# Kernel tuning notes

Measured on AMD Instinct MI355X. Metric: run time of the kernel, lower is better.

The kernel has to match this reference:

```python
import jax, jax.numpy as jnp
import numpy as np

B, N, D, H = 4, 8192, 1024, 16
C = D // H  # head dim = 64
EPS = 1e-6


def setup_inputs() -> dict:
    key = jax.random.key(0)
    ks = jax.random.split(key, 8)
    sc = 0.02
    return {
        "q": jax.random.normal(ks[0], (B, N, D), jnp.float32),
        "k": jax.random.normal(ks[1], (B, N, D), jnp.float32),
        "v": jax.random.normal(ks[2], (B, N, D), jnp.float32),
        "Wq": jax.random.normal(ks[3], (D, D), jnp.float32) * sc,
        "Wk": jax.random.normal(ks[4], (D, D), jnp.float32) * sc,
        "Wv": jax.random.normal(ks[5], (D, D), jnp.float32) * sc,
        "Wproj": jax.random.normal(ks[6], (D, D), jnp.float32) * sc,
        "focusing_factor": jnp.asarray(3.0, jnp.float32),
    }


def _to_heads(x):
    # b n (h c) -> (b h) n c
    return x.reshape(B, N, H, C).transpose(0, 2, 1, 3).reshape(B * H, N, C)


def reference(q, k, v, Wq, Wk, Wv, Wproj, focusing_factor):
    # projections (torch Linear: x @ W.T, no bias)
    qp = q @ Wq.T
    kp = k @ Wk.T
    vp = v @ Wv.T

    def feature_map(x):
        # |GELU(x)| + eps, then focused renormalization:
        # softmax(focusing_factor * log(f)) * mean(f)
        f = jnp.abs(jax.nn.gelu(x, approximate=False)) + EPS
        f_norm = f.mean(axis=-1, keepdims=True)
        return jax.nn.softmax(jnp.log(f) * focusing_factor, axis=-1) * f_norm

    qf = feature_map(qp)
    kf = feature_map(kp)

    qh = _to_heads(qf)  # [B*H, N, C]
    kh = _to_heads(kf)
    vh = _to_heads(vp)

    k_mean = kh.mean(axis=1)  # [B*H, C]
    z_inv = jnp.einsum('bnd,bd->bn', qh, k_mean) + EPS  # [B*H, N]

    # (k/sqrt(N))^T (v/sqrt(N)) == (k^T v)/N
    kv = jnp.einsum('bnc,bnd->bcd', kh, vh) / N  # [B*H, C, C]
    y = jnp.einsum('bic,bcd->bid', qh, kv) / z_inv[..., None]  # [B*H, N, C]

    y = y.reshape(B, H, N, C).transpose(0, 2, 1, 3).reshape(B, N, D)
    return y @ Wproj.T
```

## Files before the change

kernel.cpp:

```cpp
#include <hip/hip_runtime.h>

using f16 = _Float16;
typedef __attribute__((ext_vector_type(4))) _Float16 f16x4;
typedef __attribute__((ext_vector_type(8))) _Float16 f16x8;
typedef __attribute__((ext_vector_type(4))) float f32x4;

#define DEVI __device__ __forceinline__

namespace {

constexpr int BB = 4;
constexpr int NN = 8192;
constexpr int DD = 1024;
constexpr int MTOT = BB * NN;
constexpr float FSCALE = 64.0f;
constexpr float ZCONST = 64.0f * 64.0f * (8192.0f * 1e-6f);

DEVI void gl16(const void* g, void* l) {
  __builtin_amdgcn_global_load_lds(
      (__attribute__((address_space(1))) void*)(void*)g,
      (__attribute__((address_space(3))) void*)l, 16, 0, 0);
}

DEVI float wsum(float v) {
#pragma unroll
  for (int m = 32; m > 0; m >>= 1) v += __shfl_xor(v, m, 64);
  return v;
}

struct CastArgs {
  const float* src[8];
  f16* dst[8];
  int n4[8];
};

__global__ __launch_bounds__(256) void cast_kernel(CastArgs a) {
  const int z = blockIdx.y;
  const float4* __restrict__ s = (const float4*)a.src[z];
  f16x4* __restrict__ d = (f16x4*)a.dst[z];
  const int n4 = a.n4[z];
  for (int i = blockIdx.x * blockDim.x + threadIdx.x; i < n4;
       i += gridDim.x * blockDim.x) {
    float4 f = s[i];
    f16x4 o = {(f16)f.x, (f16)f.y, (f16)f.z, (f16)f.w};
    d[i] = o;
  }
}

struct Gemm3 {
  const f16* A[3];
  const f16* Bt[3];
  void* C[3];
};
struct Gemm3f {
  const float* A[3];
  const f16* Bt[3];
  f16* C[3];
};

#define GEMM_PREAMBLE()                                                      \
  constexpr int K = DD;                                                      \
  constexpr int N = DD;                                                      \
  constexpr int NKT = K / 64;                                                \
  const int nx = gridDim.x;                                                  \
  int lin = blockIdx.y * nx + blockIdx.x;                                    \
  const int cpx = (gridDim.y * nx) >> 3;                                     \
  lin = (lin & 7) * cpx + (lin >> 3);                                        \
  const size_t row0 = (size_t)(lin / nx) * 256;                              \
  const size_t col0 = (size_t)(lin % nx) * 256;                              \
  const int tid = threadIdx.x, lane = tid & 63, wv = tid >> 6;               \
  const int wm = wv >> 2, wn = wv & 3;                                       \
  const int fr = lane & 15, f7 = lane & 7, kq = lane >> 4;                   \
  const int srow = wv * 8 + (lane >> 3);                                     \
  const int ssw = (lane & 7) ^ ((lane >> 3) & 7);                            \
  const int c0e = (kq ^ f7) * 8;

__global__ __launch_bounds__(512, 2) void gemm256_fa(Gemm3f P) {
  GEMM_PREAMBLE()
  const int z = blockIdx.z;
  const float* __restrict__ A = P.A[z];
  const f16* __restrict__ Bt = P.Bt[z];
  f16* __restrict__ C = P.C[z];

  __shared__ __align__(16) f16 LA[2][2][8192];
  __shared__ __align__(16) f16 LB[2][2][8192];

  auto stageB = [&](int kts, int half) {
    const f16* src = Bt + (col0 + half * 128 + srow) * K + kts * 64 + ssw * 8;
    f16* dst = &LB[kts & 1][half][wv * 512];
#pragma unroll
    for (int c = 0; c < 2; ++c) gl16(src + (size_t)c * 64 * K, dst + c * 4096);
  };

  const int ar = tid >> 2;
  const int ac2 = (tid & 3) * 2;
  auto loadA = [&](int kts, float4* r) {
#pragma unroll
    for (int half = 0; half < 2; ++half) {
      const float* src = A + (row0 + half * 128 + ar) * (size_t)K + kts * 64;
#pragma unroll
      for (int c = 0; c < 2; ++c) {
        r[half * 4 + 2 * c + 0] = *(const float4*)(src + (ac2 + c) * 8);
        r[half * 4 + 2 * c + 1] = *(const float4*)(src + (ac2 + c) * 8 + 4);
      }
    }
  };
  auto writeA = [&](int kts, const float4* r) {
#pragma unroll
    for (int half = 0; half < 2; ++half) {
      f16* base = &LA[kts & 1][half][ar * 64];
#pragma unroll
      for (int c = 0; c < 2; ++c) {
        const float4 lo = r[half * 4 + 2 * c], hi = r[half * 4 + 2 * c + 1];
        f16x8 o = {(f16)lo.x, (f16)lo.y, (f16)lo.z, (f16)lo.w,
                   (f16)hi.x, (f16)hi.y, (f16)hi.z, (f16)hi.w};
        *(f16x8*)&base[((ac2 + c) ^ (ar & 7)) * 8] = o;
      }
    }
  };

  f32x4 acc[8][4];
#pragma unroll
  for (int i = 0; i < 8; ++i)
#pragma unroll
    for (int j = 0; j < 4; ++j) acc[i][j] = f32x4{0.f, 0.f, 0.f, 0.f};

  float4 ra[8];
  loadA(0, ra);
  stageB(0, 0); stageB(0, 1);
  asm volatile("s_waitcnt vmcnt(0)" ::: "memory");
  writeA(0, ra);
  asm volatile("s_waitcnt lgkmcnt(0)" ::: "memory");
  loadA(1, ra);
  __builtin_amdgcn_s_barrier();

  for (int kt = 0; kt < NKT; ++kt) {
    const int buf = kt & 1;
    const f16* Ah = LA[buf][wm];
    const f16* Bh = &LB[buf][wn >> 1][(wn & 1) * 4096];
    f16x8 a0[8], a1[8], b0[4], b1[4];

#pragma unroll
    for (int mi = 0; mi < 8; ++mi)
      a0[mi] = *(const f16x8*)&Ah[(mi * 16 + fr) * 64 + c0e];
#pragma unroll
    for (int ni = 0; ni < 4; ++ni)
      b0[ni] = *(const f16x8*)&Bh[(ni * 16 + fr) * 64 + c0e];
    if (kt + 1 < NKT) stageB(kt + 1, 0);
    __builtin_amdgcn_s_barrier();
    asm volatile("s_waitcnt lgkmcnt(0)" ::: "memory");
    __builtin_amdgcn_sched_barrier(0);
    __builtin_amdgcn_s_setprio(1);
#pragma unroll
    for (int mi = 0; mi < 4; ++mi)
#pragma unroll
      for (int ni = 0; ni < 4; ++ni)
        acc[mi][ni] = __builtin_amdgcn_mfma_f32_16x16x32_f16(
            a0[mi], b0[ni], acc[mi][ni], 0, 0, 0);
    __builtin_amdgcn_s_setprio(0);
    __builtin_amdgcn_s_barrier();

#pragma unroll
    for (int mi = 0; mi < 8; ++mi)
      a1[mi] = *(const f16x8*)&Ah[(mi * 16 + fr) * 64 + (c0e ^ 32)];
    if (kt + 1 < NKT) stageB(kt + 1, 1);
    __builtin_amdgcn_s_barrier();
    asm volatile("s_waitcnt lgkmcnt(0)" ::: "memory");
    __builtin_amdgcn_sched_barrier(0);
    __builtin_amdgcn_s_setprio(1);
#pragma unroll
    for (int mi = 4; mi < 8; ++mi)
#pragma unroll
      for (int ni = 0; ni < 4; ++ni)
        acc[mi][ni] = __builtin_amdgcn_mfma_f32_16x16x32_f16(
            a0[mi], b0[ni], acc[mi][ni], 0, 0, 0);
    __builtin_amdgcn_s_setprio(0);
    __builtin_amdgcn_s_barrier();

#pragma unroll
    for (int ni = 0; ni < 4; ++ni)
      b1[ni] = *(const f16x8*)&Bh[(ni * 16 + fr) * 64 + (c0e ^ 32)];
    __builtin_amdgcn_s_barrier();
    asm volatile("s_waitcnt lgkmcnt(0)" ::: "memory");
    __builtin_amdgcn_sched_barrier(0);
    __builtin_amdgcn_s_setprio(1);
#pragma unroll
    for (int mi = 0; mi < 4; ++mi)
#pragma unroll
      for (int ni = 0; ni < 4; ++ni)
        acc[mi][ni] = __builtin_amdgcn_mfma_f32_16x16x32_f16(
            a1[mi], b1[ni], acc[mi][ni], 0, 0, 0);
    __builtin_amdgcn_s_setprio(0);
    __builtin_amdgcn_s_barrier();

    __builtin_amdgcn_s_setprio(1);
#pragma unroll
    for (int mi = 4; mi < 8; ++mi)
#pragma unroll
      for (int ni = 0; ni < 4; ++ni)
        acc[mi][ni] = __builtin_amdgcn_mfma_f32_16x16x32_f16(
            a1[mi], b1[ni], acc[mi][ni], 0, 0, 0);
    __builtin_amdgcn_s_setprio(0);
    asm volatile("s_waitcnt vmcnt(0)" ::: "memory");
    __builtin_amdgcn_sched_barrier(0);
    if (kt + 1 < NKT) {
      writeA(kt + 1, ra);
      asm volatile("s_waitcnt lgkmcnt(0)" ::: "memory");
      if (kt + 2 < NKT) loadA(kt + 2, ra);
    }
    __builtin_amdgcn_s_barrier();
  }

#pragma unroll
  for (int mi = 0; mi < 8; ++mi)
#pragma unroll
    for (int ni = 0; ni < 4; ++ni) {
      const size_t colv = col0 + wn * 64 + ni * 16 + fr;
#pragma unroll
      for (int r = 0; r < 4; ++r) {
        const size_t rowv = row0 + wm * 128 + mi * 16 + (lane >> 4) * 4 + r;
        C[rowv * N + colv] = (f16)acc[mi][ni][r];
      }
    }
}

template <typename OutT>
__global__ __launch_bounds__(512, 2) void gemm256(Gemm3 P) {
  GEMM_PREAMBLE()
  const int z = blockIdx.z;
  const f16* __restrict__ A = P.A[z];
  const f16* __restrict__ Bt = P.Bt[z];
  OutT* __restrict__ C = (OutT*)P.C[z];

  __shared__ __align__(16) f16 LA[2][2][8192];
  __shared__ __align__(16) f16 LB[2][2][8192];

  auto stageA = [&](int kts, int half) {
    const f16* src = A + (row0 + half * 128 + srow) * K + kts * 64 + ssw * 8;
    f16* dst = &LA[kts & 1][half][wv * 512];
#pragma unroll
    for (int c = 0; c < 2; ++c) gl16(src + (size_t)c * 64 * K, dst + c * 4096);
  };
  auto stageB = [&](int kts, int half) {
    const f16* src = Bt + (col0 + half * 128 + srow) * K + kts * 64 + ssw * 8;
    f16* dst = &LB[kts & 1][half][wv * 512];
#pragma unroll
    for (int c = 0; c < 2; ++c) gl16(src + (size_t)c * 64 * K, dst + c * 4096);
  };

  f32x4 acc[8][4];
#pragma unroll
  for (int i = 0; i < 8; ++i)
#pragma unroll
    for (int j = 0; j < 4; ++j) acc[i][j] = f32x4{0.f, 0.f, 0.f, 0.f};

  stageA(0, 0); stageA(0, 1); stageB(0, 0); stageB(0, 1);
  stageA(1, 0); stageA(1, 1);
  asm volatile("s_waitcnt vmcnt(4)" ::: "memory");
  __builtin_amdgcn_s_barrier();

  for (int kt = 0; kt < NKT; ++kt) {
    const int buf = kt & 1;
    const f16* Ah = LA[buf][wm];
    const f16* Bh = &LB[buf][wn >> 1][(wn & 1) * 4096];
    f16x8 a0[8], a1[8], b0[4], b1[4];

#pragma unroll
    for (int mi = 0; mi < 8; ++mi)
      a0[mi] = *(const f16x8*)&Ah[(mi * 16 + fr) * 64 + c0e];
#pragma unroll
    for (int ni = 0; ni < 4; ++ni)
      b0[ni] = *(const f16x8*)&Bh[(ni * 16 + fr) * 64 + c0e];
    if (kt < NKT - 1) stageB(kt + 1, 0);
    __builtin_amdgcn_s_barrier();
    asm volatile("s_waitcnt lgkmcnt(0)" ::: "memory");
    __builtin_amdgcn_sched_barrier(0);
    __builtin_amdgcn_s_setprio(1);
#pragma unroll
    for (int mi = 0; mi < 4; ++mi)
#pragma unroll
      for (int ni = 0; ni < 4; ++ni)
        acc[mi][ni] = __builtin_amdgcn_mfma_f32_16x16x32_f16(
            a0[mi], b0[ni], acc[mi][ni], 0, 0, 0);
    __builtin_amdgcn_s_setprio(0);
    __builtin_amdgcn_s_barrier();

#pragma unroll
    for (int mi = 0; mi < 8; ++mi)
      a1[mi] = *(const f16x8*)&Ah[(mi * 16 + fr) * 64 + (c0e ^ 32)];
    if (kt < NKT - 1) stageB(kt + 1, 1);
    __builtin_amdgcn_s_barrier();
    asm volatile("s_waitcnt lgkmcnt(0)" ::: "memory");
    __builtin_amdgcn_sched_barrier(0);
    __builtin_amdgcn_s_setprio(1);
#pragma unroll
    for (int mi = 4; mi < 8; ++mi)
#pragma unroll
      for (int ni = 0; ni < 4; ++ni)
        acc[mi][ni] = __builtin_amdgcn_mfma_f32_16x16x32_f16(
            a0[mi], b0[ni], acc[mi][ni], 0, 0, 0);
    __builtin_amdgcn_s_setprio(0);
    __builtin_amdgcn_s_barrier();

#pragma unroll
    for (int ni = 0; ni < 4; ++ni)
      b1[ni] = *(const f16x8*)&Bh[(ni * 16 + fr) * 64 + (c0e ^ 32)];
    if (kt < NKT - 2) stageA(kt + 2, 0);
    __builtin_amdgcn_s_barrier();
    asm volatile("s_waitcnt lgkmcnt(0)" ::: "memory");
    __builtin_amdgcn_sched_barrier(0);
    __builtin_amdgcn_s_setprio(1);
#pragma unroll
    for (int mi = 0; mi < 4; ++mi)
#pragma unroll
      for (int ni = 0; ni < 4; ++ni)
        acc[mi][ni] = __builtin_amdgcn_mfma_f32_16x16x32_f16(
            a1[mi], b1[ni], acc[mi][ni], 0, 0, 0);
    __builtin_amdgcn_s_setprio(0);
    __builtin_amdgcn_s_barrier();

    if (kt < NKT - 2) stageA(kt + 2, 1);
    __builtin_amdgcn_s_barrier();
    __builtin_amdgcn_s_setprio(1);
#pragma unroll
    for (int mi = 4; mi < 8; ++mi)
#pragma unroll
      for (int ni = 0; ni < 4; ++ni)
        acc[mi][ni] = __builtin_amdgcn_mfma_f32_16x16x32_f16(
            a1[mi], b1[ni], acc[mi][ni], 0, 0, 0);
    __builtin_amdgcn_s_setprio(0);
    if (kt < NKT - 2)
      asm volatile("s_waitcnt vmcnt(4)" ::: "memory");
    else
      asm volatile("s_waitcnt vmcnt(0)" ::: "memory");
    __builtin_amdgcn_s_barrier();
  }

#pragma unroll
  for (int mi = 0; mi < 8; ++mi)
#pragma unroll
    for (int ni = 0; ni < 4; ++ni) {
      const size_t colv = col0 + wn * 64 + ni * 16 + fr;
#pragma unroll
      for (int r = 0; r < 4; ++r) {
        const size_t rowv = row0 + wm * 128 + mi * 16 + (lane >> 4) * 4 + r;
        C[rowv * N + colv] = (OutT)acc[mi][ni][r];
      }
    }
}

__global__ __launch_bounds__(256) void feature_kernel(
    const f16* __restrict__ qp, const f16* __restrict__ kp,
    f16* __restrict__ qf, f16* __restrict__ kf, const float* __restrict__ ffp) {
  const int lane = threadIdx.x & 63;
  const size_t row = (size_t)blockIdx.x * 4 + (threadIdx.x >> 6);
  const bool isq = (blockIdx.y == 0);
  const f16* __restrict__ src = isq ? qp : kp;
  f16* __restrict__ dst = isq ? qf : kf;
  const float ff = ffp[0];

  const f16x8* p = (const f16x8*)(src + row * DD + lane * 16);
  f16x8 v0 = p[0], v1 = p[1];

  float f0[16];
  float ps = 0.f;
#pragma unroll
  for (int j = 0; j < 16; ++j) {
    const float x = (float)(j < 8 ? v0[j] : v1[j - 8]);
    const float ax = fabsf(x) * 0.70710678118654752f;
    const float tt = 1.0f / (1.0f + 0.3275911f * ax);
    const float poly =
        tt * (0.254829592f +
              tt * (-0.284496736f +
                    tt * (1.421413741f +
                          tt * (-1.453152027f + tt * 1.061405429f))));
    const float erfv = 1.0f - poly * __expf(-ax * ax);
    const float g = 0.5f * x * (1.0f + copysignf(erfv, x));
    const float fv = fabsf(g) + 1e-6f;
    f0[j] = fv;
    ps += fv;
  }
  const float fsum = wsum(ps);

  float e[16];
  float es = 0.f;
#pragma unroll
  for (int j = 0; j < 16; ++j) {
    e[j] = __expf(ff * __logf(f0[j]));
    es += e[j];
  }
  const float esum = wsum(es);

  const float scale = fsum * (1.0f / 1024.0f) / esum * FSCALE;
  f16x8 o0, o1;
#pragma unroll
  for (int j = 0; j < 8; ++j) {
    o0[j] = (f16)(e[j] * scale);
    o1[j] = (f16)(e[j + 8] * scale);
  }
  f16x8* q = (f16x8*)(dst + row * DD + lane * 16);
  q[0] = o0;
  q[1] = o1;
}

__global__ __launch_bounds__(256) void kv_kernel(
    const f16* __restrict__ kf, const f16* __restrict__ vp,
    float* __restrict__ kvsum, float* __restrict__ colsum) {
  const int bh = blockIdx.x;
  const int b = bh >> 4, h = bh & 15;
  const int tid = threadIdx.x, lane = tid & 63, wave = tid >> 6;
  __shared__ __align__(16) f16 kt[32 * 64];
  __shared__ __align__(16) f16 vt[32 * 64];
  __shared__ float csred[4][64];

  f32x4 acc[4];
#pragma unroll
  for (int ni = 0; ni < 4; ++ni) acc[ni] = f32x4{0.f, 0.f, 0.f, 0.f};
  float cpart = 0.f;

  const int srow = wave * 8 + (lane >> 3);
  const int scol = (lane & 7) * 8;
  const int colbase = h * 64;
  const int n0base = blockIdx.y * 512;

  for (int n0 = n0base; n0 < n0base + 512; n0 += 32) {
    const size_t gofs = ((size_t)(b * NN + n0 + srow)) * DD + colbase + scol;
    gl16(kf + gofs, &kt[wave * 512]);
    gl16(vp + gofs, &vt[wave * 512]);
    __syncthreads();
    {
      const int c = tid & 63;
      const int r0 = (tid >> 6) * 8;
#pragma unroll
      for (int rr = 0; rr < 8; ++rr) cpart += (float)kt[(r0 + rr) * 64 + c];
    }
    f16x8 a, bfr[4];
#pragma unroll
    for (int j = 0; j < 8; ++j)
      a[j] = kt[((lane >> 4) * 8 + j) * 64 + wave * 16 + (lane & 15)];
#pragma unroll
    for (int ni = 0; ni < 4; ++ni)
#pragma unroll
      for (int j = 0; j < 8; ++j)
        bfr[ni][j] = vt[((lane >> 4) * 8 + j) * 64 + ni * 16 + (lane & 15)];
#pragma unroll
    for (int ni = 0; ni < 4; ++ni)
      acc[ni] = __builtin_amdgcn_mfma_f32_16x16x32_f16(a, bfr[ni], acc[ni], 0, 0, 0);
    __syncthreads();
  }
#pragma unroll
  for (int ni = 0; ni < 4; ++ni)
#pragma unroll
    for (int r = 0; r < 4; ++r) {
      const int c = wave * 16 + (lane >> 4) * 4 + r;
      const int d = ni * 16 + (lane & 15);
      atomicAdd(&kvsum[(size_t)bh * 4096 + c * 64 + d], acc[ni][r]);
    }
  csred[tid >> 6][tid & 63] = cpart;
  __syncthreads();
  if (tid < 64)
    atomicAdd(&colsum[bh * 64 + tid],
              csred[0][tid] + csred[1][tid] + csred[2][tid] + csred[3][tid]);
}

__global__ __launch_bounds__(256) void y_kernel(
    const f16* __restrict__ qf, const f16* __restrict__ kv16,
    const float* __restrict__ colsum, f16* __restrict__ y) {
  const int bh = blockIdx.x, b = bh >> 4, h = bh & 15;
  const int n0 = blockIdx.y * 128;
  const int tid = threadIdx.x, lane = tid & 63, wave = tid >> 6;
  __shared__ __align__(16) f16 qs[128 * 64];
  __shared__ __align__(16) f16 kvs[64 * 64];
  __shared__ float cs[64];
  __shared__ float zr[128];

#pragma unroll
  for (int cc = 0; cc < 4; ++cc) {
    const int r = wave * 32 + cc * 8 + (lane >> 3);
    gl16(qf + ((size_t)(b * NN + n0 + r)) * DD + h * 64 + (lane & 7) * 8,
         &qs[(wave * 4 + cc) * 512]);
  }
#pragma unroll
  for (int cc = 0; cc < 2; ++cc) {
    const int r = wave * 16 + cc * 8 + (lane >> 3);
    gl16(kv16 + (size_t)bh * 4096 + r * 64 + (lane & 7) * 8,
         &kvs[(wave * 2 + cc) * 512]);
  }
  if (tid < 64) cs[tid] = colsum[bh * 64 + tid];
  __syncthreads();
  if (tid < 128) {
    float zv = 0.f;
    for (int cc = 0; cc < 64; ++cc) {
      const int c = (cc + tid) & 63;
      zv += (float)qs[tid * 64 + c] * cs[c];
    }
    zr[tid] = zv + ZCONST;
  }
  __syncthreads();

  f32x4 acc[2][4];
#pragma unroll
  for (int mi = 0; mi < 2; ++mi)
#pragma unroll
    for (int ni = 0; ni < 4; ++ni) acc[mi][ni] = f32x4{0.f, 0.f, 0.f, 0.f};

#pragma unroll
  for (int ks = 0; ks < 2; ++ks) {
    f16x8 a[2], bfr[4];
#pragma unroll
    for (int mi = 0; mi < 2; ++mi)
      a[mi] = *(const f16x8*)&qs[(wave * 32 + mi * 16 + (lane & 15)) * 64 +
                                 ks * 32 + (lane >> 4) * 8];
#pragma unroll
    for (int ni = 0; ni < 4; ++ni)
#pragma unroll
      for (int j = 0; j < 8; ++j)
        bfr[ni][j] = kvs[(ks * 32 + (lane >> 4) * 8 + j) * 64 + ni * 16 + (lane & 15)];
#pragma unroll
    for (int mi = 0; mi < 2; ++mi)
#pragma unroll
      for (int ni = 0; ni < 4; ++ni)
        acc[mi][ni] = __builtin_amdgcn_mfma_f32_16x16x32_f16(
            a[mi], bfr[ni], acc[mi][ni], 0, 0, 0);
  }
#pragma unroll
  for (int mi = 0; mi < 2; ++mi)
#pragma unroll
    for (int ni = 0; ni < 4; ++ni)
#pragma unroll
      for (int r = 0; r < 4; ++r) {
        const int rrow = wave * 32 + mi * 16 + (lane >> 4) * 4 + r;
        const int d = ni * 16 + (lane & 15);
        const float yv = acc[mi][ni][r] / zr[rrow];
        y[((size_t)(b * NN + n0 + rrow)) * DD + h * 64 + d] = (f16)yv;
      }
}

}

extern "C" void kernel_launch(void* const* d_in, const int* in_sizes, int n_in,
                              void* d_out, int out_size, void* d_ws, size_t ws_size,
                              hipStream_t stream) {
  const float* q = (const float*)d_in[0];
  const float* k = (const float*)d_in[1];
  const float* v = (const float*)d_in[2];
  const float* Wq = (const float*)d_in[3];
  const float* Wk = (const float*)d_in[4];
  const float* Wv = (const float*)d_in[5];
  const float* Wp = (const float*)d_in[6];
  const float* ffp = (const float*)d_in[7];

  char* w = (char*)d_ws;
  size_t off = 0;
  auto alloc = [&](size_t b) {
    void* p = (void*)(w + off);
    off += (b + 255) & ~(size_t)255;
    return p;
  };
  const size_t big = (size_t)MTOT * DD * sizeof(f16);
  f16* qp16 = (f16*)alloc(big);
  f16* kp16 = (f16*)alloc(big);
  f16* vp16 = (f16*)alloc(big);
  f16* qf  = (f16*)alloc(big);
  f16* kf  = (f16*)alloc(big);
  f16* y16 = (f16*)alloc(big);
  f16* Wq16 = (f16*)alloc((size_t)DD * DD * 2);
  f16* Wk16 = (f16*)alloc((size_t)DD * DD * 2);
  f16* Wv16 = (f16*)alloc((size_t)DD * DD * 2);
  f16* Wp16 = (f16*)alloc((size_t)DD * DD * 2);
  float* kvsum = (float*)alloc(64 * 64 * 64 * sizeof(float));
  float* colsum = (float*)alloc(64 * 64 * sizeof(float));
  f16* kv16 = (f16*)alloc(64 * 64 * 64 * sizeof(f16));
  if (off > ws_size) return;

  CastArgs ca{};
  ca.src[0] = Wq; ca.dst[0] = Wq16; ca.n4[0] = DD * DD / 4;
  ca.src[1] = Wk; ca.dst[1] = Wk16; ca.n4[1] = DD * DD / 4;
  ca.src[2] = Wv; ca.dst[2] = Wv16; ca.n4[2] = DD * DD / 4;
  ca.src[3] = Wp; ca.dst[3] = Wp16; ca.n4[3] = DD * DD / 4;
  cast_kernel<<<dim3(128, 4), 256, 0, stream>>>(ca);

  Gemm3f gp{};
  gp.A[0] = q; gp.Bt[0] = Wq16; gp.C[0] = qp16;
  gp.A[1] = k; gp.Bt[1] = Wk16; gp.C[1] = kp16;
  gp.A[2] = v; gp.Bt[2] = Wv16; gp.C[2] = vp16;
  gemm256_fa<<<dim3(DD / 256, MTOT / 256, 3), 512, 0, stream>>>(gp);

  feature_kernel<<<dim3(MTOT / 4, 2), 256, 0, stream>>>(qp16, kp16, qf, kf, ffp);

  hipMemsetAsync(kvsum, 0, 64 * 64 * 64 * sizeof(float) + 64 * 64 * sizeof(float),
                 stream);
  kv_kernel<<<dim3(64, 16), 256, 0, stream>>>(kf, vp16, kvsum, colsum);

  CastArgs cb{};
  cb.src[0] = kvsum; cb.dst[0] = kv16; cb.n4[0] = 64 * 64 * 64 / 4;
  cast_kernel<<<dim3(64, 1), 256, 0, stream>>>(cb);

  y_kernel<<<dim3(64, 64), 256, 0, stream>>>(qf, kv16, colsum, y16);

  Gemm3 gf{};
  gf.A[0] = y16; gf.Bt[0] = Wp16; gf.C[0] = d_out;
  gemm256<float><<<dim3(DD / 256, MTOT / 256, 1), 512, 0, stream>>>(gf);
}
```

Baseline: 585.7 us.

## Fold kv into output projection and fuse normalization into final GEMM

Drops the separate y-computation pass and the kv cast. Each batch's per-head kv matrices are premultiplied with Wproj into a per-batch fused matrix M, and the final GEMM reads qf directly. The z normalization (dot of q with colsum) is computed in registers while the A tile is staged into shared memory. This removes writing and re-reading the full y tensor and one kernel launch. In exchange, A loads now go through registers instead of direct-to-LDS copies, with a full vmcnt wait each iteration, which may weaken overlap; fp16 scaling by SC is added to keep values in range.

```diff
diff --git a/kernel.cpp b/kernel.cpp
--- a/kernel.cpp
+++ b/kernel.cpp
@@ -15,6 +15,7 @@
 constexpr int MTOT = BB * NN;
 constexpr float FSCALE = 64.0f;
 constexpr float ZCONST = 64.0f * 64.0f * (8192.0f * 1e-6f);
+constexpr float SC = 4096.0f;
 
 DEVI void gl16(const void* g, void* l) {
   __builtin_amdgcn_global_load_lds(
@@ -29,9 +30,9 @@
 }
 
 struct CastArgs {
-  const float* src[8];
-  f16* dst[8];
-  int n4[8];
+  const float* src[4];
+  f16* dst[4];
+  int n4[4];
 };
 
 __global__ __launch_bounds__(256) void cast_kernel(CastArgs a) {
@@ -47,15 +48,16 @@
   }
 }
 
-struct Gemm3 {
-  const f16* A[3];
-  const f16* Bt[3];
-  void* C[3];
-};
 struct Gemm3f {
   const float* A[3];
   const f16* Bt[3];
   f16* C[3];
+};
+struct GemmZf {
+  const f16* A;
+  const f16* M;
+  const float* colsum;
+  float* C;
 };
 
 #define GEMM_PREAMBLE()                                                      \
@@ -224,23 +226,16 @@
     }
 }
 
-template <typename OutT>
-__global__ __launch_bounds__(512, 2) void gemm256(Gemm3 P) {
+__global__ __launch_bounds__(512, 2) void gemm256_zf(GemmZf P) {
   GEMM_PREAMBLE()
-  const int z = blockIdx.z;
-  const f16* __restrict__ A = P.A[z];
-  const f16* __restrict__ Bt = P.Bt[z];
-  OutT* __restrict__ C = (OutT*)P.C[z];
+  const f16* __restrict__ A = P.A;
+  float* __restrict__ C = P.C;
+  const int batch = (int)(row0 >> 13);
+  const f16* __restrict__ Bt = P.M + (size_t)batch * DD * DD;
 
   __shared__ __align__(16) f16 LA[2][2][8192];
   __shared__ __align__(16) f16 LB[2][2][8192];
 
-  auto stageA = [&](int kts, int half) {
-    const f16* src = A + (row0 + half * 128 + srow) * K + kts * 64 + ssw * 8;
-    f16* dst = &LA[kts & 1][half][wv * 512];
-#pragma unroll
-    for (int c = 0; c < 2; ++c) gl16(src + (size_t)c * 64 * K, dst + c * 4096);
-  };
   auto stageB = [&](int kts, int half) {
     const f16* src = Bt + (col0 + half * 128 + srow) * K + kts * 64 + ssw * 8;
     f16* dst = &LB[kts & 1][half][wv * 512];
@@ -248,15 +243,66 @@
     for (int c = 0; c < 2; ++c) gl16(src + (size_t)c * 64 * K, dst + c * 4096);
   };
 
+  const int ar = tid >> 2;
+  const int ac2 = (tid & 3) * 2;
+  f16x8 ra[4];
+  float csr[16];
+
+  auto loadA = [&](int kts) {
+#pragma unroll
+    for (int half = 0; half < 2; ++half) {
+      const f16* src =
+          A + (row0 + half * 128 + ar) * (size_t)K + kts * 64 + ac2 * 8;
+      ra[half * 2 + 0] = *(const f16x8*)(src);
+      ra[half * 2 + 1] = *(const f16x8*)(src + 8);
+    }
+  };
+  auto loadCS = [&](int head) {
+    const float* cs = P.colsum + ((batch << 4) + head) * 64 + ac2 * 8;
+#pragma unroll
+    for (int j = 0; j < 16; ++j) csr[j] = cs[j];
+  };
+  auto writeA = [&](int kts) {
+#pragma unroll
+    for (int half = 0; half < 2; ++half) {
+      float xv[16];
+      float dot = 0.f;
+#pragma unroll
+      for (int c = 0; c < 2; ++c)
+#pragma unroll
+        for (int j = 0; j < 8; ++j) {
+          const float x = (float)ra[half * 2 + c][j];
+          xv[c * 8 + j] = x;
+          dot += x * csr[c * 8 + j];
+        }
+      dot += __shfl_xor(dot, 1, 64);
+      dot += __shfl_xor(dot, 2, 64);
+      const float s = SC / (dot + ZCONST);
+      f16* base = &LA[kts & 1][half][ar * 64];
+#pragma unroll
+      for (int c = 0; c < 2; ++c) {
+        f16x8 o;
+#pragma unroll
+        for (int j = 0; j < 8; ++j) o[j] = (f16)(xv[c * 8 + j] * s);
+        *(f16x8*)&base[((ac2 + c) ^ (ar & 7)) * 8] = o;
+      }
+    }
+  };
+
   f32x4 acc[8][4];
 #pragma unroll
   for (int i = 0; i < 8; ++i)
 #pragma unroll
     for (int j = 0; j < 4; ++j) acc[i][j] = f32x4{0.f, 0.f, 0.f, 0.f};
 
-  stageA(0, 0); stageA(0, 1); stageB(0, 0); stageB(0, 1);
-  stageA(1, 0); stageA(1, 1);
-  asm volatile("s_waitcnt vmcnt(4)" ::: "memory");
+  loadA(0);
+  stageB(0, 0); stageB(0, 1);
+  loadCS(0);
+  asm volatile("s_waitcnt vmcnt(0)" ::: "memory");
+  writeA(0);
+  asm volatile("s_waitcnt lgkmcnt(0)" ::: "memory");
+  loadA(1);
+  loadCS(1);
   __builtin_amdgcn_s_barrier();
 
   for (int kt = 0; kt < NKT; ++kt) {
@@ -271,7 +317,7 @@
 #pragma unroll
     for (int ni = 0; ni < 4; ++ni)
       b0[ni] = *(const f16x8*)&Bh[(ni * 16 + fr) * 64 + c0e];
-    if (kt < NKT - 1) stageB(kt + 1, 0);
+    if (kt + 1 < NKT) stageB(kt + 1, 0);
     __builtin_amdgcn_s_barrier();
     asm volatile("s_waitcnt lgkmcnt(0)" ::: "memory");
     __builtin_amdgcn_sched_barrier(0);
@@ -288,7 +334,7 @@
 #pragma unroll
     for (int mi = 0; mi < 8; ++mi)
       a1[mi] = *(const f16x8*)&Ah[(mi * 16 + fr) * 64 + (c0e ^ 32)];
-    if (kt < NKT - 1) stageB(kt + 1, 1);
+    if (kt + 1 < NKT) stageB(kt + 1, 1);
     __builtin_amdgcn_s_barrier();
     asm volatile("s_waitcnt lgkmcnt(0)" ::: "memory");
     __builtin_amdgcn_sched_barrier(0);
@@ -305,7 +351,6 @@
 #pragma unroll
     for (int ni = 0; ni < 4; ++ni)
       b1[ni] = *(const f16x8*)&Bh[(ni * 16 + fr) * 64 + (c0e ^ 32)];
-    if (kt < NKT - 2) stageA(kt + 2, 0);
     __builtin_amdgcn_s_barrier();
     asm volatile("s_waitcnt lgkmcnt(0)" ::: "memory");
     __builtin_amdgcn_sched_barrier(0);
@@ -319,8 +364,6 @@
     __builtin_amdgcn_s_setprio(0);
     __builtin_amdgcn_s_barrier();
 
-    if (kt < NKT - 2) stageA(kt + 2, 1);
-    __builtin_amdgcn_s_barrier();
     __builtin_amdgcn_s_setprio(1);
 #pragma unroll
     for (int mi = 4; mi < 8; ++mi)
@@ -329,10 +372,13 @@
         acc[mi][ni] = __builtin_amdgcn_mfma_f32_16x16x32_f16(
             a1[mi], b1[ni], acc[mi][ni], 0, 0, 0);
     __builtin_amdgcn_s_setprio(0);
-    if (kt < NKT - 2)
-      asm volatile("s_waitcnt vmcnt(4)" ::: "memory");
-    else
-      asm volatile("s_waitcnt vmcnt(0)" ::: "memory");
+    asm volatile("s_waitcnt vmcnt(0)" ::: "memory");
+    __builtin_amdgcn_sched_barrier(0);
+    if (kt + 1 < NKT) {
+      writeA(kt + 1);
+      asm volatile("s_waitcnt lgkmcnt(0)" ::: "memory");
+      if (kt + 2 < NKT) { loadA(kt + 2); loadCS(kt + 2); }
+    }
     __builtin_amdgcn_s_barrier();
   }
 
@@ -344,7 +390,7 @@
 #pragma unroll
       for (int r = 0; r < 4; ++r) {
         const size_t rowv = row0 + wm * 128 + mi * 16 + (lane >> 4) * 4 + r;
-        C[rowv * N + colv] = (OutT)acc[mi][ni][r];
+        C[rowv * N + colv] = acc[mi][ni][r];
       }
     }
 }
@@ -463,77 +509,36 @@
               csred[0][tid] + csred[1][tid] + csred[2][tid] + csred[3][tid]);
 }
 
-__global__ __launch_bounds__(256) void y_kernel(
-    const f16* __restrict__ qf, const f16* __restrict__ kv16,
-    const float* __restrict__ colsum, f16* __restrict__ y) {
+__global__ __launch_bounds__(256) void mprep_kernel(
+    const float* __restrict__ kvsum, const float* __restrict__ Wp,
+    f16* __restrict__ M) {
   const int bh = blockIdx.x, b = bh >> 4, h = bh & 15;
-  const int n0 = blockIdx.y * 128;
-  const int tid = threadIdx.x, lane = tid & 63, wave = tid >> 6;
-  __shared__ __align__(16) f16 qs[128 * 64];
-  __shared__ __align__(16) f16 kvs[64 * 64];
-  __shared__ float cs[64];
-  __shared__ float zr[128];
-
-#pragma unroll
-  for (int cc = 0; cc < 4; ++cc) {
-    const int r = wave * 32 + cc * 8 + (lane >> 3);
-    gl16(qf + ((size_t)(b * NN + n0 + r)) * DD + h * 64 + (lane & 7) * 8,
-         &qs[(wave * 4 + cc) * 512]);
-  }
-#pragma unroll
-  for (int cc = 0; cc < 2; ++cc) {
-    const int r = wave * 16 + cc * 8 + (lane >> 3);
-    gl16(kv16 + (size_t)bh * 4096 + r * 64 + (lane & 7) * 8,
-         &kvs[(wave * 2 + cc) * 512]);
-  }
-  if (tid < 64) cs[tid] = colsum[bh * 64 + tid];
+  const int tid = threadIdx.x;
+  __shared__ float kvs[64 * 64];
+#pragma unroll
+  for (int j = 0; j < 4; ++j)
+    ((float4*)kvs)[tid * 4 + j] =
+        ((const float4*)(kvsum + (size_t)bh * 4096))[tid * 4 + j];
   __syncthreads();
-  if (tid < 128) {
-    float zv = 0.f;
-    for (int cc = 0; cc < 64; ++cc) {
-      const int c = (cc + tid) & 63;
-      zv += (float)qs[tid * 64 + c] * cs[c];
-    }
-    zr[tid] = zv + ZCONST;
-  }
-  __syncthreads();
-
-  f32x4 acc[2][4];
-#pragma unroll
-  for (int mi = 0; mi < 2; ++mi)
-#pragma unroll
-    for (int ni = 0; ni < 4; ++ni) acc[mi][ni] = f32x4{0.f, 0.f, 0.f, 0.f};
-
-#pragma unroll
-  for (int ks = 0; ks < 2; ++ks) {
-    f16x8 a[2], bfr[4];
-#pragma unroll
-    for (int mi = 0; mi < 2; ++mi)
-      a[mi] = *(const f16x8*)&qs[(wave * 32 + mi * 16 + (lane & 15)) * 64 +
-                                 ks * 32 + (lane >> 4) * 8];
-#pragma unroll
-    for (int ni = 0; ni < 4; ++ni)
-#pragma unroll
-      for (int j = 0; j < 8; ++j)
-        bfr[ni][j] = kvs[(ks * 32 + (lane >> 4) * 8 + j) * 64 + ni * 16 + (lane & 15)];
-#pragma unroll
-    for (int mi = 0; mi < 2; ++mi)
-#pragma unroll
-      for (int ni = 0; ni < 4; ++ni)
-        acc[mi][ni] = __builtin_amdgcn_mfma_f32_16x16x32_f16(
-            a[mi], bfr[ni], acc[mi][ni], 0, 0, 0);
-  }
-#pragma unroll
-  for (int mi = 0; mi < 2; ++mi)
-#pragma unroll
-    for (int ni = 0; ni < 4; ++ni)
-#pragma unroll
-      for (int r = 0; r < 4; ++r) {
-        const int rrow = wave * 32 + mi * 16 + (lane >> 4) * 4 + r;
-        const int d = ni * 16 + (lane & 15);
-        const float yv = acc[mi][ni][r] / zr[rrow];
-        y[((size_t)(b * NN + n0 + rrow)) * DD + h * 64 + d] = (f16)yv;
-      }
+
+  const int dp = blockIdx.y * 256 + tid;
+  float wr[64];
+#pragma unroll
+  for (int j = 0; j < 16; ++j)
+    *(float4*)&wr[j * 4] =
+        *(const float4*)(Wp + (size_t)dp * DD + h * 64 + j * 4);
+
+  f16 out[64];
+#pragma unroll 4
+  for (int c = 0; c < 64; ++c) {
+    float s = 0.f;
+#pragma unroll
+    for (int d = 0; d < 64; ++d) s += kvs[c * 64 + d] * wr[d];
+    out[c] = (f16)(s * (1.0f / SC));
+  }
+  f16* dst = M + (size_t)b * DD * DD + (size_t)dp * DD + h * 64;
+#pragma unroll
+  for (int j = 0; j < 8; ++j) ((f16x8*)dst)[j] = ((f16x8*)out)[j];
 }
 
 }
@@ -563,22 +568,21 @@
   f16* vp16 = (f16*)alloc(big);
   f16* qf  = (f16*)alloc(big);
   f16* kf  = (f16*)alloc(big);
-  f16* y16 = (f16*)alloc(big);
+  f16* M   = (f16*)alloc((size_t)BB * DD * DD * sizeof(f16));
   f16* Wq16 = (f16*)alloc((size_t)DD * DD * 2);
   f16* Wk16 = (f16*)alloc((size_t)DD * DD * 2);
   f16* Wv16 = (f16*)alloc((size_t)DD * DD * 2);
-  f16* Wp16 = (f16*)alloc((size_t)DD * DD * 2);
   float* kvsum = (float*)alloc(64 * 64 * 64 * sizeof(float));
   float* colsum = (float*)alloc(64 * 64 * sizeof(float));
-  f16* kv16 = (f16*)alloc(64 * 64 * 64 * sizeof(f16));
   if (off > ws_size) return;
 
   CastArgs ca{};
   ca.src[0] = Wq; ca.dst[0] = Wq16; ca.n4[0] = DD * DD / 4;
   ca.src[1] = Wk; ca.dst[1] = Wk16; ca.n4[1] = DD * DD / 4;
   ca.src[2] = Wv; ca.dst[2] = Wv16; ca.n4[2] = DD * DD / 4;
-  ca.src[3] = Wp; ca.dst[3] = Wp16; ca.n4[3] = DD * DD / 4;
-  cast_kernel<<<dim3(128, 4), 256, 0, stream>>>(ca);
+  cast_kernel<<<dim3(128, 3), 256, 0, stream>>>(ca);
+  hipMemsetAsync(kvsum, 0, 64 * 64 * 64 * sizeof(float) + 64 * 64 * sizeof(float),
+                 stream);
 
   Gemm3f gp{};
   gp.A[0] = q; gp.Bt[0] = Wq16; gp.C[0] = qp16;
@@ -588,17 +592,11 @@
 
   feature_kernel<<<dim3(MTOT / 4, 2), 256, 0, stream>>>(qp16, kp16, qf, kf, ffp);
 
-  hipMemsetAsync(kvsum, 0, 64 * 64 * 64 * sizeof(float) + 64 * 64 * sizeof(float),
-                 stream);
   kv_kernel<<<dim3(64, 16), 256, 0, stream>>>(kf, vp16, kvsum, colsum);
 
-  CastArgs cb{};
-  cb.src[0] = kvsum; cb.dst[0] = kv16; cb.n4[0] = 64 * 64 * 64 / 4;
-  cast_kernel<<<dim3(64, 1), 256, 0, stream>>>(cb);
-
-  y_kernel<<<dim3(64, 64), 256, 0, stream>>>(qf, kv16, colsum, y16);
-
-  Gemm3 gf{};
-  gf.A[0] = y16; gf.Bt[0] = Wp16; gf.C[0] = d_out;
-  gemm256<float><<<dim3(DD / 256, MTOT / 256, 1), 512, 0, stream>>>(gf);
-}
+  mprep_kernel<<<dim3(64, 4), 256, 0, stream>>>(kvsum, Wp, M);
+
+  GemmZf gz{};
+  gz.A = qf; gz.M = M; gz.colsum = colsum; gz.C = (float*)d_out;
+  gemm256_zf<<<dim3(DD / 256, MTOT / 256, 1), 512, 0, stream>>>(gz);
+}
```

Measured after the change: 599.8 us. +2.4%, slower.
